# Performance work log

Measured on AMD Instinct MI355X. Metric: run time of the kernel, lower is better.

## Reference

```python
import jax, jax.numpy as jnp
import numpy as np

D_MODEL = 1024
N_HEADS = 16
BLOCK = 256
NEG = -1e9


def setup_inputs() -> dict:
    key = jax.random.key(0)
    ks = jax.random.split(key, 5)
    B, S, D = 4, 4096, D_MODEL
    scale = 0.02
    inp = {
        "x": jax.random.normal(ks[0], (B, S, D), dtype=jnp.float32),
        "Wq": jax.random.normal(ks[1], (D, D), dtype=jnp.float32) * scale,
        "bq": jnp.zeros((D,), dtype=jnp.float32),
        "Wk": jax.random.normal(ks[2], (D, D), dtype=jnp.float32) * scale,
        "bk": jnp.zeros((D,), dtype=jnp.float32),
        "Wv": jax.random.normal(ks[3], (D, D), dtype=jnp.float32) * scale,
        "bv": jnp.zeros((D,), dtype=jnp.float32),
        "Wo": jax.random.normal(ks[4], (D, D), dtype=jnp.float32) * scale,
        "bo": jnp.zeros((D,), dtype=jnp.float32),
    }
    return inp


def _local_attention(x, Wq, bq, Wk, bk, Wv, bv, Wo, bo):
    B, S, D = x.shape
    h, dh, bs = N_HEADS, D // N_HEADS, BLOCK
    pad_len = (bs - S % bs) % bs
    if pad_len > 0:
        x = jnp.pad(x, ((0, 0), (0, pad_len), (0, 0)))
    Sp = x.shape[1]
    nb = Sp // bs
    # independent local blocks: [B*nb, bs, D]
    xb = x.reshape(B * nb, bs, D)

    def proj(W, b):
        # [N, bs, D] -> [N, h, bs, dh]
        y = xb @ W + b
        return y.reshape(B * nb, bs, h, dh).transpose(0, 2, 1, 3)

    q = proj(Wq, bq)
    k = proj(Wk, bk)
    v = proj(Wv, bv)

    scores = jnp.einsum('nhqd,nhkd->nhqk', q, k) / jnp.sqrt(jnp.asarray(dh, x.dtype))
    causal = jnp.tril(jnp.ones((bs, bs), dtype=bool))  # block-local causal mask
    scores = jnp.where(causal, scores, jnp.asarray(NEG, x.dtype))
    probs = jax.nn.softmax(scores, axis=-1)
    out = jnp.einsum('nhqk,nhkd->nhqd', probs, v)
    out = out.transpose(0, 2, 1, 3).reshape(B, Sp, D)
    if pad_len > 0:
        out = out[:, :S, :]
    return out @ Wo + bo


def reference(x, Wq, bq, Wk, bk, Wv, bv, Wo, bo):
    return _local_attention(x, Wq, bq, Wk, bk, Wv, bv, Wo, bo)
```

## Files before the change

### kernel.cpp

```cpp
#include <hip/hip_runtime.h>
#include <cstdint>
#include <cstddef>

typedef unsigned short u16;
typedef __attribute__((ext_vector_type(8))) short s16x8;
typedef __attribute__((ext_vector_type(8))) unsigned short u16x8;
typedef __attribute__((ext_vector_type(4))) unsigned short u16x4;
typedef __attribute__((ext_vector_type(4))) float f32x4;

#define D_MODEL 1024
#define DH 64
#define BS 256

__device__ __forceinline__ u16 f2bf(float f) {
  union { float f; unsigned int i; } x; x.f = f;
  unsigned int r = x.i + 0x7fffu + ((x.i >> 16) & 1u);
  return (u16)(r >> 16);
}

__device__ __forceinline__ void gl_lds16(const u16* g, u16* l) {
  __builtin_amdgcn_global_load_lds((const __attribute__((address_space(1))) void*)g,
                                   (__attribute__((address_space(3))) void*)l, 16, 0, 0);
}

__device__ __forceinline__ unsigned lds_off(const u16* p) {
  return (unsigned)(uintptr_t)(const __attribute__((address_space(3))) u16*)p;
}

__global__ __launch_bounds__(256) void cast_x(const float* __restrict__ x, u16* __restrict__ xb) {
  int i = (blockIdx.x * 256 + threadIdx.x) * 8;
  f32x4 a0 = *(const f32x4*)(x + i);
  f32x4 a1 = *(const f32x4*)(x + i + 4);
  u16x8 v;
#pragma unroll
  for (int j = 0; j < 4; ++j) { v[j] = f2bf(a0[j]); v[j + 4] = f2bf(a1[j]); }
  *(u16x8*)(xb + i) = v;
}

__global__ __launch_bounds__(256) void transpose_w(const float* __restrict__ w0,
                                                   const float* __restrict__ w1,
                                                   const float* __restrict__ w2,
                                                   const float* __restrict__ w3,
                                                   u16* __restrict__ out) {
  __shared__ u16 tile[64][65];
  const int z = blockIdx.z;
  const float* W = (z == 0) ? w0 : (z == 1) ? w1 : (z == 2) ? w2 : w3;
  u16* O = out + (size_t)z * (D_MODEL * D_MODEL);
  const int kb = blockIdx.y * 64, nb = blockIdx.x * 64;
  const int t = threadIdx.x;
#pragma unroll
  for (int i = 0; i < 16; ++i) {
    int e = i * 256 + t;
    int r = e >> 6, c = e & 63;
    tile[r][c] = f2bf(W[(size_t)(kb + r) * D_MODEL + nb + c]);
  }
  __syncthreads();
#pragma unroll
  for (int i = 0; i < 16; ++i) {
    int e = i * 256 + t;
    int r = e >> 6, c = e & 63;
    O[(size_t)(nb + r) * D_MODEL + kb + c] = tile[c][r];
  }
}


#define TIU 16384
#define HIU 8192

__device__ __forceinline__ void stage_half(const u16* __restrict__ src, int rowG0, int k0,
                                           u16* ldst, int tid) {
#pragma unroll
  for (int i = 0; i < 2; ++i) {
    int c = i * 512 + tid;
    int cs = c ^ ((c >> 3) & 7);
    gl_lds16(src + (size_t)(rowG0 + (cs >> 3)) * D_MODEL + k0 + (cs & 7) * 8,
             ldst + c * 8);
  }
}

#define NOPX ((void)0)
#define BARX() __builtin_amdgcn_s_barrier()
#define VMW(N) asm volatile("s_waitcnt vmcnt(" #N ")" ::: "memory")
#define SBAR() __builtin_amdgcn_sched_barrier(0)
#define LGK8() asm volatile("s_waitcnt lgkmcnt(8)")

#define DSR128(dst, b, off) asm volatile("ds_read_b128 %0, %1 offset:" #off : "=v"(dst) : "v"(b))

#define LDA8(P, MH) do { \
  const unsigned _o = (P) * 32768u + (MH) * 8192u; \
  DSR128(a[0][0], aK0 + _o, 0);    DSR128(a[0][1], aK1 + _o, 0); \
  DSR128(a[1][0], aK0 + _o, 2048); DSR128(a[1][1], aK1 + _o, 2048); \
  DSR128(a[2][0], aK0 + _o, 4096); DSR128(a[2][1], aK1 + _o, 4096); \
  DSR128(a[3][0], aK0 + _o, 6144); DSR128(a[3][1], aK1 + _o, 6144); \
} while (0)

#define LDB4(P, NH) do { \
  const unsigned _o = (P) * 32768u + (NH) * 4096u; \
  DSR128(b[NH][0][0], bK0 + _o, 0);    DSR128(b[NH][0][1], bK1 + _o, 0); \
  DSR128(b[NH][1][0], bK0 + _o, 2048); DSR128(b[NH][1][1], bK1 + _o, 2048); \
} while (0)

#define MF16(MH, NH) do { \
  __builtin_amdgcn_s_setprio(1); \
  _Pragma("unroll") for (int kk = 0; kk < 2; ++kk) \
  _Pragma("unroll") for (int mt = 0; mt < 4; ++mt) \
  _Pragma("unroll") for (int nt = 0; nt < 2; ++nt) \
    acc[(MH) * 4 + mt][(NH) * 2 + nt] = __builtin_amdgcn_mfma_f32_16x16x32_bf16( \
        a[mt][kk], b[NH][nt][kk], acc[(MH) * 4 + mt][(NH) * 2 + nt], 0, 0, 0); \
  __builtin_amdgcn_s_setprio(0); \
} while (0)

#define STA(T, H) stage_half(A, rowBase + (H) * 128, (T) * 64, As + ((T) & 1) * TIU + (H) * HIU, t)
#define STB(T, H) stage_half(W, colBase + (H) * 128, (T) * 64, Bs + ((T) & 1) * TIU + (H) * HIU, t)

#define PWAIT() do { BARX(); asm volatile("s_waitcnt lgkmcnt(0)"); SBAR(); } while (0)

#define KTILE(P, S1, S2, S3, S4, WAIT) do { \
  LDA8(P, 0); LDB4(P, 0); S1; LGK8(); PWAIT();  MF16(0, 0); BARX(); \
  LDB4(P, 1);             S2; PWAIT();          MF16(0, 1); BARX(); \
  LDA8(P, 1);             S3; PWAIT();          MF16(1, 1); BARX(); \
                    S4; WAIT; BARX(); SBAR();   MF16(1, 0); BARX(); \
} while (0)

template <int MODE, int NCB>
__global__ __launch_bounds__(512, 2) void gemm8(
    const u16* __restrict__ A, const u16* __restrict__ W,
    const float* __restrict__ b0, const float* __restrict__ b1, const float* __restrict__ b2,
    void* __restrict__ o0, void* __restrict__ o1, void* __restrict__ o2) {
  __shared__ u16 As[2 * TIU];
  __shared__ u16 Bs[2 * TIU];

  const int nwg = gridDim.x;
  const int wg = blockIdx.x;
  const int swz = (wg & 7) * (nwg >> 3) + (wg >> 3);
  const int rowBase = (swz / NCB) * 256;
  const int colBase = (swz % NCB) * 256;

  const int t = threadIdx.x;
  const int wave = t >> 6, lane = t & 63, l15 = lane & 15, q4 = lane >> 4;
  const int wm = wave >> 2, wn = wave & 3;
  const int arow = wm * 128 + l15;
  const int brow = wn * 64 + l15;

  const unsigned swzc = (unsigned)((q4 ^ (l15 & 7)) << 4);
  const unsigned aK0 = lds_off(As) + (unsigned)arow * 128u + swzc;
  const unsigned aK1 = aK0 ^ 64u;
  const unsigned bK0 = lds_off(Bs) + (unsigned)brow * 128u + swzc;
  const unsigned bK1 = bK0 ^ 64u;

  f32x4 acc[8][4];
#pragma unroll
  for (int i = 0; i < 8; ++i)
#pragma unroll
    for (int j = 0; j < 4; ++j) acc[i][j] = {0.f, 0.f, 0.f, 0.f};

  s16x8 a[4][2];
  s16x8 b[2][2][2];

  STB(0, 0); STB(0, 1); STA(0, 0); STA(0, 1);
  VMW(4);
  STB(1, 0); STB(1, 1); STA(1, 0);
  VMW(6);
  BARX();

#pragma unroll 1
  for (int tg = 0; tg < 14; tg += 2) {
    KTILE(0, STA(tg + 1, 1), STB(tg + 2, 0), STB(tg + 2, 1), STA(tg + 2, 0), VMW(6));
    KTILE(1, STA(tg + 2, 1), STB(tg + 3, 0), STB(tg + 3, 1), STA(tg + 3, 0), VMW(6));
  }
  KTILE(0, STA(15, 1), NOPX, NOPX, NOPX, VMW(0));
  KTILE(1, NOPX, NOPX, NOPX, NOPX, NOPX);

  if constexpr (MODE == 0) {
    const int z = colBase >> 10;
    const int colL = (colBase & 1023) + wn * 64;
    if (z < 2) {
      const float* bias = (z == 0) ? b0 : b1;
      u16* Out = (u16*)((z == 0) ? o0 : o1);
      float bv[4];
#pragma unroll
      for (int ni = 0; ni < 4; ++ni) bv[ni] = bias[colL + ni * 16 + l15];
#pragma unroll
      for (int mi = 0; mi < 8; ++mi) {
#pragma unroll
        for (int r = 0; r < 4; ++r) {
          size_t row = (size_t)(rowBase + wm * 128 + mi * 16 + q4 * 4 + r);
#pragma unroll
          for (int ni = 0; ni < 4; ++ni)
            Out[row * D_MODEL + colL + ni * 16 + l15] = f2bf(acc[mi][ni][r] + bv[ni]);
        }
      }
    } else {
      u16* Vt = (u16*)o2;
      const int nIdx = rowBase >> 8;
      float bv[4];
#pragma unroll
      for (int ni = 0; ni < 4; ++ni) bv[ni] = b2[colL + ni * 16 + l15];
#pragma unroll
      for (int mi = 0; mi < 8; ++mi) {
        const int tk = wm * 128 + mi * 16 + q4 * 4;
#pragma unroll
        for (int ni = 0; ni < 4; ++ni) {
          const int col = colL + ni * 16 + l15;
          u16x4 v4;
#pragma unroll
          for (int r = 0; r < 4; ++r) v4[r] = f2bf(acc[mi][ni][r] + bv[ni]);
          *(u16x4*)(Vt + (((size_t)nIdx * 16 + (col >> 6)) * 64 + (col & 63)) * 256 + tk) = v4;
        }
      }
    }
  } else {
    float* Out = (float*)o0;
    const int colL = colBase + wn * 64;
    float bv[4];
#pragma unroll
    for (int ni = 0; ni < 4; ++ni) bv[ni] = b0[colL + ni * 16 + l15];
#pragma unroll
    for (int mi = 0; mi < 8; ++mi) {
#pragma unroll
      for (int r = 0; r < 4; ++r) {
        size_t row = (size_t)(rowBase + wm * 128 + mi * 16 + q4 * 4 + r);
#pragma unroll
        for (int ni = 0; ni < 4; ++ni)
          Out[row * D_MODEL + colL + ni * 16 + l15] = acc[mi][ni][r] + bv[ni];
      }
    }
  }
}

__global__ __launch_bounds__(256, 3) void attn(const u16* __restrict__ Q, const u16* __restrict__ K,
                                               const u16* __restrict__ Vt, u16* __restrict__ O) {
  __shared__ u16 pl[4 * 16 * 264];
  const int g = blockIdx.x;
  const int nh = g >> 1, j = g & 1;
  const int n = nh >> 4, h = nh & 15;
  const size_t base = (size_t)n * BS * D_MODEL + (size_t)h * DH;
  const u16* Qb = Q + base;
  const u16* Kb = K + base;
  const u16* Vb = Vt + (size_t)nh * (64 * 256);
  u16* Ob = O + base;
  const int t = threadIdx.x, wave = t >> 6, lane = t & 63, l15 = lane & 15, q4 = lane >> 4;
  const int slot = j * 4 + wave;
  u16* pw = pl + wave * 16 * 264;

#pragma unroll 1
  for (int pi = 0; pi < 2; ++pi) {
    const int a = pi ? (15 - slot) : slot;
    const int r0 = a * 16;

    s16x8 aq[2];
#pragma unroll
    for (int kk = 0; kk < 2; ++kk)
      aq[kk] = *(const s16x8*)(Qb + (size_t)(r0 + l15) * D_MODEL + kk * 32 + q4 * 8);

    f32x4 sc[16];
#pragma unroll
    for (int i = 0; i < 16; ++i) sc[i] = {0.f, 0.f, 0.f, 0.f};

    __builtin_amdgcn_s_setprio(1);
#pragma unroll
    for (int nt = 0; nt < 16; ++nt) {
      if (nt <= a) {
#pragma unroll
        for (int kk = 0; kk < 2; ++kk) {
          s16x8 bk = *(const s16x8*)(Kb + (size_t)(nt * 16 + l15) * D_MODEL + kk * 32 + q4 * 8);
          sc[nt] = __builtin_amdgcn_mfma_f32_16x16x32_bf16(aq[kk], bk, sc[nt], 0, 0, 0);
        }
      }
    }
    __builtin_amdgcn_s_setprio(0);

    float mrow[4] = {-3e38f, -3e38f, -3e38f, -3e38f};
#pragma unroll
    for (int nt = 0; nt < 16; ++nt) {
      if (nt <= a) {
#pragma unroll
        for (int r = 0; r < 4; ++r) {
          int col = nt * 16 + l15;
          int row = r0 + q4 * 4 + r;
          float s = (col > row) ? -1.0e9f : sc[nt][r] * 0.125f;
          sc[nt][r] = s;
          mrow[r] = fmaxf(mrow[r], s);
        }
      }
    }
#pragma unroll
    for (int r = 0; r < 4; ++r)
#pragma unroll
      for (int off = 1; off < 16; off <<= 1)
        mrow[r] = fmaxf(mrow[r], __shfl_xor(mrow[r], off, 64));

    float lrow[4] = {0.f, 0.f, 0.f, 0.f};
#pragma unroll
    for (int nt = 0; nt < 16; ++nt) {
      if (nt <= a) {
#pragma unroll
        for (int r = 0; r < 4; ++r) {
          float e = exp2f((sc[nt][r] - mrow[r]) * 1.44269504f);
          sc[nt][r] = e;
          lrow[r] += e;
        }
      }
    }
#pragma unroll
    for (int r = 0; r < 4; ++r)
#pragma unroll
      for (int off = 1; off < 16; off <<= 1)
        lrow[r] += __shfl_xor(lrow[r], off, 64);

#pragma unroll
    for (int nt = 0; nt < 16; ++nt) {
      if (nt <= a) {
#pragma unroll
        for (int r = 0; r < 4; ++r)
          pw[(q4 * 4 + r) * 264 + nt * 16 + l15] = f2bf(sc[nt][r]);
      }
    }
    if ((a & 1) == 0) {
#pragma unroll
      for (int r = 0; r < 4; ++r)
        pw[(q4 * 4 + r) * 264 + (a + 1) * 16 + l15] = 0;
    }
    const int ktmax = (a + 2) >> 1;

    f32x4 oc[4];
#pragma unroll
    for (int i = 0; i < 4; ++i) oc[i] = {0.f, 0.f, 0.f, 0.f};
    __builtin_amdgcn_s_setprio(1);
#pragma unroll
    for (int kt = 0; kt < 8; ++kt) {
      if (kt < ktmax) {
        s16x8 ap = *(const s16x8*)(pw + l15 * 264 + kt * 32 + q4 * 8);
#pragma unroll
        for (int dt = 0; dt < 4; ++dt) {
          s16x8 bv = *(const s16x8*)(Vb + (size_t)(dt * 16 + l15) * 256 + kt * 32 + q4 * 8);
          oc[dt] = __builtin_amdgcn_mfma_f32_16x16x32_bf16(ap, bv, oc[dt], 0, 0, 0);
        }
      }
    }
    __builtin_amdgcn_s_setprio(0);

    float inv[4];
#pragma unroll
    for (int r = 0; r < 4; ++r) inv[r] = 1.0f / lrow[r];

#pragma unroll
    for (int dt = 0; dt < 4; ++dt)
#pragma unroll
      for (int r = 0; r < 4; ++r)
        pw[(q4 * 4 + r) * 264 + dt * 16 + l15] = f2bf(oc[dt][r] * inv[r]);
#pragma unroll
    for (int k = 0; k < 2; ++k) {
      int c2 = k * 64 + lane;
      int row = c2 >> 3, c8 = (c2 & 7) * 8;
      u16x8 v = *(const u16x8*)(pw + row * 264 + c8);
      *(u16x8*)(Ob + (size_t)(r0 + row) * D_MODEL + c8) = v;
    }
  }
}

extern "C" void kernel_launch(void* const* d_in, const int* in_sizes, int n_in,
                              void* d_out, int out_size, void* d_ws, size_t ws_size,
                              hipStream_t stream) {
  const float* x  = (const float*)d_in[0];
  const float* Wq = (const float*)d_in[1];
  const float* bq = (const float*)d_in[2];
  const float* Wk = (const float*)d_in[3];
  const float* bk = (const float*)d_in[4];
  const float* Wv = (const float*)d_in[5];
  const float* bv = (const float*)d_in[6];
  const float* Wo = (const float*)d_in[7];
  const float* bo = (const float*)d_in[8];
  float* out = (float*)d_out;

  u16* ws = (u16*)d_ws;
  u16* Wt = ws;
  u16* Xb = ws + (size_t)4 * 1048576;
  u16* Qw = Xb + (size_t)16777216;
  u16* Kw = Qw + (size_t)16777216;
  u16* Vw = Kw + (size_t)16777216;
  u16* Ow = Qw;

  cast_x<<<dim3(8192), 256, 0, stream>>>(x, Xb);
  transpose_w<<<dim3(16, 16, 4), 256, 0, stream>>>(Wq, Wk, Wv, Wo, Wt);
  gemm8<0, 12><<<dim3(768), 512, 0, stream>>>(Xb, Wt, bq, bk, bv, Qw, Kw, Vw);
  attn<<<dim3(2048), 256, 0, stream>>>(Qw, Kw, Vw, Ow);
  gemm8<1, 4><<<dim3(256), 512, 0, stream>>>(Ow, Wt + (size_t)3 * 1048576, bo,
                                             nullptr, nullptr, out, nullptr, nullptr);
}
```

Measured before the change: 411.2 us.

## Stage K/V in swizzled LDS per head and keep P in registers

The attention kernel now runs one 512-thread block per (block, head). It stages the whole K tile and transposed V tile into swizzled shared memory, so eight waves share those loads instead of each re-reading K and V from global memory. The score MFMA is computed transposed (K as A operand), so each lane owns a query column. Softmax reductions then shrink to two cross-quad shuffles, and the bf16 probabilities feed the 16x16x16 MFMA directly from registers, removing the LDS round-trip for P and for the output. The cost is 64 KB of LDS per block, which may limit occupancy, and it relies on the stage_half and HIU helpers defined elsewhere.

```diff
diff --git a/kernel.cpp b/kernel.cpp
--- a/kernel.cpp
+++ b/kernel.cpp
@@ -4,6 +4,7 @@
 
 typedef unsigned short u16;
 typedef __attribute__((ext_vector_type(8))) short s16x8;
+typedef __attribute__((ext_vector_type(4))) short s16x4;
 typedef __attribute__((ext_vector_type(8))) unsigned short u16x8;
 typedef __attribute__((ext_vector_type(4))) unsigned short u16x4;
 typedef __attribute__((ext_vector_type(4))) float f32x4;
@@ -25,6 +26,15 @@
 
 __device__ __forceinline__ unsigned lds_off(const u16* p) {
   return (unsigned)(uintptr_t)(const __attribute__((address_space(3))) u16*)p;
+}
+
+__device__ __forceinline__ f32x4 mfma16(s16x4 a, s16x4 b, f32x4 c) {
+#if __has_builtin(__builtin_amdgcn_mfma_f32_16x16x16bf16_1k)
+  return __builtin_amdgcn_mfma_f32_16x16x16bf16_1k(a, b, c, 0, 0, 0);
+#else
+  asm("v_mfma_f32_16x16x16_bf16 %0, %1, %2, %0" : "+v"(c) : "v"(a), "v"(b));
+  return c;
+#endif
 }
 
 __global__ __launch_bounds__(256) void cast_x(const float* __restrict__ x, u16* __restrict__ xb) {
@@ -228,30 +238,42 @@
   }
 }
 
-__global__ __launch_bounds__(256, 3) void attn(const u16* __restrict__ Q, const u16* __restrict__ K,
+__global__ __launch_bounds__(512, 4) void attn(const u16* __restrict__ Q, const u16* __restrict__ K,
                                                const u16* __restrict__ Vt, u16* __restrict__ O) {
-  __shared__ u16 pl[4 * 16 * 264];
-  const int g = blockIdx.x;
-  const int nh = g >> 1, j = g & 1;
+  __shared__ u16 Ks[256 * 64];
+  __shared__ u16 Vs[64 * 256];
+  const int nh = blockIdx.x;
   const int n = nh >> 4, h = nh & 15;
   const size_t base = (size_t)n * BS * D_MODEL + (size_t)h * DH;
   const u16* Qb = Q + base;
   const u16* Kb = K + base;
-  const u16* Vb = Vt + (size_t)nh * (64 * 256);
+  const u16* Vg = Vt + (size_t)nh * (64 * 256);
   u16* Ob = O + base;
   const int t = threadIdx.x, wave = t >> 6, lane = t & 63, l15 = lane & 15, q4 = lane >> 4;
-  const int slot = j * 4 + wave;
-  u16* pw = pl + wave * 16 * 264;
+
+  stage_half(Kb, 0, 0, Ks, t);
+  stage_half(Kb, 128, 0, Ks + HIU, t);
+#pragma unroll
+  for (int i = 0; i < 4; ++i) {
+    int c = i * 512 + t;
+    int d = c >> 5, s = c & 31;
+    gl_lds16(Vg + d * 256 + (s ^ (d & 7)) * 8, Vs + c * 8);
+  }
+  __syncthreads();
+
+  const int kswz = ((q4 << 3) ^ ((l15 & 7) << 3));
+  const int vswz = (l15 & 7) << 3;
 
 #pragma unroll 1
   for (int pi = 0; pi < 2; ++pi) {
-    const int a = pi ? (15 - slot) : slot;
+    const int a = pi ? (15 - wave) : wave;
     const int r0 = a * 16;
+    const int qg = r0 + l15;
 
     s16x8 aq[2];
 #pragma unroll
     for (int kk = 0; kk < 2; ++kk)
-      aq[kk] = *(const s16x8*)(Qb + (size_t)(r0 + l15) * D_MODEL + kk * 32 + q4 * 8);
+      aq[kk] = *(const s16x8*)(Qb + (size_t)qg * D_MODEL + kk * 32 + q4 * 8);
 
     f32x4 sc[16];
 #pragma unroll
@@ -263,98 +285,70 @@
       if (nt <= a) {
 #pragma unroll
         for (int kk = 0; kk < 2; ++kk) {
-          s16x8 bk = *(const s16x8*)(Kb + (size_t)(nt * 16 + l15) * D_MODEL + kk * 32 + q4 * 8);
-          sc[nt] = __builtin_amdgcn_mfma_f32_16x16x32_bf16(aq[kk], bk, sc[nt], 0, 0, 0);
+          s16x8 ak = *(const s16x8*)(Ks + (nt * 16 + l15) * 64 + (kswz ^ (kk << 5)));
+          sc[nt] = __builtin_amdgcn_mfma_f32_16x16x32_bf16(ak, aq[kk], sc[nt], 0, 0, 0);
         }
       }
     }
     __builtin_amdgcn_s_setprio(0);
 
-    float mrow[4] = {-3e38f, -3e38f, -3e38f, -3e38f};
+    float m = -3e38f;
 #pragma unroll
     for (int nt = 0; nt < 16; ++nt) {
       if (nt <= a) {
 #pragma unroll
         for (int r = 0; r < 4; ++r) {
-          int col = nt * 16 + l15;
-          int row = r0 + q4 * 4 + r;
-          float s = (col > row) ? -1.0e9f : sc[nt][r] * 0.125f;
+          int kg = nt * 16 + q4 * 4 + r;
+          float s = (kg > qg) ? -1.0e9f : sc[nt][r] * 0.125f;
           sc[nt][r] = s;
-          mrow[r] = fmaxf(mrow[r], s);
-        }
-      }
-    }
-#pragma unroll
-    for (int r = 0; r < 4; ++r)
-#pragma unroll
-      for (int off = 1; off < 16; off <<= 1)
-        mrow[r] = fmaxf(mrow[r], __shfl_xor(mrow[r], off, 64));
-
-    float lrow[4] = {0.f, 0.f, 0.f, 0.f};
+          m = fmaxf(m, s);
+        }
+      }
+    }
+    m = fmaxf(m, __shfl_xor(m, 16, 64));
+    m = fmaxf(m, __shfl_xor(m, 32, 64));
+
+    float l = 0.f;
+    s16x4 pa[16];
 #pragma unroll
     for (int nt = 0; nt < 16; ++nt) {
       if (nt <= a) {
+        s16x4 p;
 #pragma unroll
         for (int r = 0; r < 4; ++r) {
-          float e = exp2f((sc[nt][r] - mrow[r]) * 1.44269504f);
-          sc[nt][r] = e;
-          lrow[r] += e;
-        }
-      }
-    }
-#pragma unroll
-    for (int r = 0; r < 4; ++r)
-#pragma unroll
-      for (int off = 1; off < 16; off <<= 1)
-        lrow[r] += __shfl_xor(lrow[r], off, 64);
-
+          float e = exp2f((sc[nt][r] - m) * 1.44269504f);
+          l += e;
+          p[r] = (short)f2bf(e);
+        }
+        pa[nt] = p;
+      }
+    }
+    l += __shfl_xor(l, 16, 64);
+    l += __shfl_xor(l, 32, 64);
+
+    f32x4 oc[4];
+#pragma unroll
+    for (int i = 0; i < 4; ++i) oc[i] = {0.f, 0.f, 0.f, 0.f};
+    __builtin_amdgcn_s_setprio(1);
 #pragma unroll
     for (int nt = 0; nt < 16; ++nt) {
       if (nt <= a) {
 #pragma unroll
-        for (int r = 0; r < 4; ++r)
-          pw[(q4 * 4 + r) * 264 + nt * 16 + l15] = f2bf(sc[nt][r]);
-      }
-    }
-    if ((a & 1) == 0) {
-#pragma unroll
-      for (int r = 0; r < 4; ++r)
-        pw[(q4 * 4 + r) * 264 + (a + 1) * 16 + l15] = 0;
-    }
-    const int ktmax = (a + 2) >> 1;
-
-    f32x4 oc[4];
-#pragma unroll
-    for (int i = 0; i < 4; ++i) oc[i] = {0.f, 0.f, 0.f, 0.f};
-    __builtin_amdgcn_s_setprio(1);
-#pragma unroll
-    for (int kt = 0; kt < 8; ++kt) {
-      if (kt < ktmax) {
-        s16x8 ap = *(const s16x8*)(pw + l15 * 264 + kt * 32 + q4 * 8);
-#pragma unroll
         for (int dt = 0; dt < 4; ++dt) {
-          s16x8 bv = *(const s16x8*)(Vb + (size_t)(dt * 16 + l15) * 256 + kt * 32 + q4 * 8);
-          oc[dt] = __builtin_amdgcn_mfma_f32_16x16x32_bf16(ap, bv, oc[dt], 0, 0, 0);
+          s16x4 av = *(const s16x4*)(Vs + (dt * 16 + l15) * 256 + ((nt * 16 + q4 * 4) ^ vswz));
+          oc[dt] = mfma16(av, pa[nt], oc[dt]);
         }
       }
     }
     __builtin_amdgcn_s_setprio(0);
 
-    float inv[4];
-#pragma unroll
-    for (int r = 0; r < 4; ++r) inv[r] = 1.0f / lrow[r];
-
-#pragma unroll
-    for (int dt = 0; dt < 4; ++dt)
-#pragma unroll
-      for (int r = 0; r < 4; ++r)
-        pw[(q4 * 4 + r) * 264 + dt * 16 + l15] = f2bf(oc[dt][r] * inv[r]);
-#pragma unroll
-    for (int k = 0; k < 2; ++k) {
-      int c2 = k * 64 + lane;
-      int row = c2 >> 3, c8 = (c2 & 7) * 8;
-      u16x8 v = *(const u16x8*)(pw + row * 264 + c8);
-      *(u16x8*)(Ob + (size_t)(r0 + row) * D_MODEL + c8) = v;
+    const float inv = 1.0f / l;
+#pragma unroll
+    for (int dt = 0; dt < 4; ++dt) {
+      u16x4 v;
+#pragma unroll
+      for (int r = 0; r < 4; ++r) v[r] = f2bf(oc[dt][r] * inv);
+      *(u16x4*)(Ob + (size_t)qg * D_MODEL + dt * 16 + q4 * 4) = v;
     }
   }
 }
@@ -384,7 +378,7 @@
   cast_x<<<dim3(8192), 256, 0, stream>>>(x, Xb);
   transpose_w<<<dim3(16, 16, 4), 256, 0, stream>>>(Wq, Wk, Wv, Wo, Wt);
   gemm8<0, 12><<<dim3(768), 512, 0, stream>>>(Xb, Wt, bq, bk, bv, Qw, Kw, Vw);
-  attn<<<dim3(2048), 256, 0, stream>>>(Qw, Kw, Vw, Ow);
+  attn<<<dim3(1024), 512, 0, stream>>>(Qw, Kw, Vw, Ow);
   gemm8<1, 4><<<dim3(256), 512, 0, stream>>>(Ow, Wt + (size_t)3 * 1048576, bo,
                                              nullptr, nullptr, out, nullptr, nullptr);
 }
```

Measured after the change: 336.5 us. 1.22x faster.
